# Optimization experiments

Measured on AMD Instinct MI355X. Metric: run time of the kernel, lower is better.

## Reference

```python
import jax, jax.numpy as jnp
import numpy as np
from jax import lax

PRE_NMS = 2000
POST_NMS = 300
NMS_THRESH = 0.7
MIN_SIZE = 16.0
SCALE = 1.0
RATIOS = (0.5, 1.0, 2.0)
SCALES = (8, 16, 32)
STRIDES = (8, 16, 32)
FEAT_HW = ((100, 100), (50, 50), (25, 25))
BASE_SIZE = 16.0


def _anchor_base(scale):
    py = px = BASE_SIZE / 2.0
    ab = np.zeros((len(RATIOS), 4), dtype=np.float32)
    for i, r in enumerate(RATIOS):
        h = BASE_SIZE * scale * np.sqrt(r)
        w = BASE_SIZE * scale * np.sqrt(1.0 / r)
        ab[i] = [py - h / 2.0, px - w / 2.0, py + h / 2.0, px + w / 2.0]
    return ab


def _enum_anchors():
    out = []
    for lvl in range(3):
        ab = _anchor_base(SCALES[lvl])
        hh, ww = FEAT_HW[lvl]
        fs = STRIDES[lvl]
        sy = np.arange(0, hh * fs, fs)
        sx = np.arange(0, ww * fs, fs)
        sx, sy = np.meshgrid(sx, sy)
        shift = np.stack((sy.ravel(), sx.ravel(), sy.ravel(), sx.ravel()), axis=1)
        a = ab[None, :, :] + shift[:, None, :]  # [K, A, 4]
        out.append(a.reshape(-1, 4).astype(np.float32))
    return np.concatenate(out, axis=0)  # [39375, 4]


def setup_inputs() -> dict:
    key = jax.random.key(0)
    ks = jax.random.split(key, 8)
    inp = {
        "feat0": jax.random.normal(ks[0], (2, 256, 100, 100), jnp.float32),
        "feat1": jax.random.normal(ks[1], (2, 256, 50, 50), jnp.float32),
        "feat2": jax.random.normal(ks[2], (2, 256, 25, 25), jnp.float32),
        "conv_w": 0.01 * jax.random.normal(ks[3], (256, 256, 3, 3), jnp.float32),
        "conv_b": jnp.zeros((256,), jnp.float32),
        "score_w": 0.01 * jax.random.normal(ks[4], (6, 256), jnp.float32),
        "score_b": jnp.zeros((6,), jnp.float32),
        "loc_w": 0.01 * jax.random.normal(ks[5], (12, 256), jnp.float32),
        "loc_b": jnp.zeros((12,), jnp.float32),
        "anchors": jnp.asarray(_enum_anchors()),
        "img_h": 800,
        "img_w": 800,
    }
    return inp


def loc2bbox(anchors, loc):
    src_h = anchors[:, 2] - anchors[:, 0]
    src_w = anchors[:, 3] - anchors[:, 1]
    ctr_y = anchors[:, 0] + 0.5 * src_h
    ctr_x = anchors[:, 1] + 0.5 * src_w
    dy, dx, dh, dw = loc[:, 0], loc[:, 1], loc[:, 2], loc[:, 3]
    cy = dy * src_h + ctr_y
    cx = dx * src_w + ctr_x
    h = jnp.exp(dh) * src_h
    w = jnp.exp(dw) * src_w
    return jnp.stack([cy - 0.5 * h, cx - 0.5 * w, cy + 0.5 * h, cx + 0.5 * w], axis=1)


def _iou_matrix(boxes):
    area = (boxes[:, 2] - boxes[:, 0]) * (boxes[:, 3] - boxes[:, 1])
    tl = jnp.maximum(boxes[:, None, :2], boxes[None, :, :2])
    br = jnp.minimum(boxes[:, None, 2:], boxes[None, :, 2:])
    wh = jnp.clip(br - tl, 0.0)
    inter = wh[..., 0] * wh[..., 1]
    return inter / (area[:, None] + area[None, :] - inter + 1e-12)


def _nms_keep(boxes, valid):
    # greedy NMS over score-sorted boxes; returns boolean keep mask
    M = _iou_matrix(boxes)  # [PRE_NMS, PRE_NMS]
    idx = jnp.arange(PRE_NMS)

    def body(i, suppressed):
        sup_later = (~suppressed[i]) & (M[i] > NMS_THRESH) & (idx > i)
        return suppressed | sup_later

    suppressed = lax.fori_loop(0, PRE_NMS, body, ~valid)
    return ~suppressed


def _propose(loc, fg, anchors, img_h, img_w):
    roi = loc2bbox(anchors, loc)  # [S, 4]
    roi = jnp.stack([
        jnp.clip(roi[:, 0], 0.0, float(img_h)),
        jnp.clip(roi[:, 1], 0.0, float(img_w)),
        jnp.clip(roi[:, 2], 0.0, float(img_h)),
        jnp.clip(roi[:, 3], 0.0, float(img_w)),
    ], axis=1)
    hs = roi[:, 2] - roi[:, 0]
    ws = roi[:, 3] - roi[:, 1]
    valid = (hs >= MIN_SIZE * SCALE) & (ws >= MIN_SIZE * SCALE)
    sc = jnp.where(valid, fg, -jnp.inf)
    top_sc, top_idx = lax.top_k(sc, PRE_NMS)
    boxes = roi[top_idx]
    keep = _nms_keep(boxes, jnp.isfinite(top_sc))
    # stable move of kept boxes to the front (indices are unique)
    order = jnp.argsort(jnp.where(keep, jnp.arange(PRE_NMS), PRE_NMS))[:POST_NMS]
    rois = boxes[order] * keep[order][:, None].astype(boxes.dtype)  # zero-pad invalid
    return rois  # [POST_NMS, 4]


def reference(feat0, feat1, feat2, conv_w, conv_b, score_w, score_b, loc_w, loc_b, anchors, img_h, img_w):
    feats = [feat0, feat1, feat2]
    n = feat0.shape[0]
    locs, scores, fgs = [], [], []
    dn = ("NCHW", "OIHW", "NCHW")
    for x in feats:
        h = jax.nn.relu(
            lax.conv_general_dilated(x, conv_w, (1, 1), "SAME", dimension_numbers=dn)
            + conv_b[None, :, None, None]
        )
        hh, ww = h.shape[2], h.shape[3]
        loc = jnp.einsum("nchw,oc->nhwo", h, loc_w) + loc_b  # [n,h,w,12]
        sc = jnp.einsum("nchw,oc->nhwo", h, score_w) + score_b  # [n,h,w,6]
        fg = jax.nn.softmax(sc.reshape(n, hh, ww, 3, 2), axis=-1)[..., 1]
        locs.append(loc.reshape(n, -1, 4))
        scores.append(sc.reshape(n, -1, 2))
        fgs.append(fg.reshape(n, -1))
    rpn_locs = jnp.concatenate(locs, axis=1)      # [n, S, 4]
    rpn_scores = jnp.concatenate(scores, axis=1)  # [n, S, 2]
    rpn_fg = jnp.concatenate(fgs, axis=1)         # [n, S]
    rois = jax.vmap(lambda l, f: _propose(l, f, anchors, img_h, img_w))(rpn_locs, rpn_fg)
    rois = rois.reshape(-1, 4)  # [n*POST_NMS, 4]
    roi_indices = jnp.repeat(jnp.arange(n, dtype=jnp.int32), POST_NMS)
    return rpn_locs, rpn_scores, rois, roi_indices, anchors
```

## Files before the change

kernel.cpp:

```cpp
#include <hip/hip_runtime.h>
#include <hip/hip_fp16.h>
#include <cstdint>
#include <cstddef>

typedef unsigned long long u64;
typedef unsigned int u32;
typedef __attribute__((ext_vector_type(8))) _Float16 f16x8;
typedef __attribute__((ext_vector_type(4))) float f32x4;

#define NANCHORS 39375
#define PRE_NMS  2000
#define POST_NMS 300
#define CAND_CAP 4096
#define MPAD 2048
#define UNEG 0x007FFFFFu

__device__ __forceinline__ u32 f2u(float f) {
  u32 u = __float_as_uint(f);
  return (u & 0x80000000u) ? ~u : (u | 0x80000000u);
}

#define GLOAD16(gp, lp) __builtin_amdgcn_global_load_lds( \
    (const __attribute__((address_space(1))) u32*)(const void*)(gp), \
    (__attribute__((address_space(3))) u32*)(void*)(lp), 16, 0, 0)

__global__ __launch_bounds__(256) void xsplit_kernel(
    const float* __restrict__ f0, const float* __restrict__ f1, const float* __restrict__ f2,
    short* __restrict__ xh, short* __restrict__ xl)
{
  __shared__ float tile[64][65];
  int t = blockIdx.x;
  int HW, W, W2, np; const float* fp; int AB, ABS;
  if (t < 1256)      { HW = 10000; W = 100; W2 = 102; np = 157; fp = f0; AB = 0;       ABS = 2663424; }
  else if (t < 1576) { t -= 1256; HW = 2500; W = 50; W2 = 52; np = 40; fp = f1; AB = 5326848; ABS = 692224; }
  else               { t -= 1576; HW = 625;  W = 25; W2 = 27; np = 10; fp = f2; AB = 6711296; ABS = 186624; }
  int posb = t % np, r = t / np;
  int ci0 = (r & 3) * 64, b = r >> 2;
  int pos0 = posb * 64;
  int tid = threadIdx.x, lane = tid & 63, w = tid >> 6;
  int rp = pos0 + lane; if (rp >= HW) rp = HW - 1;
  const float* src = fp + (size_t)(b * 256 + ci0) * HW;
#pragma unroll
  for (int p = 0; p < 16; ++p) {
    int cl = w * 16 + p;
    tile[cl][lane] = src[(size_t)cl * HW + rp];
  }
  __syncthreads();
  int pix = tid >> 2, cq = tid & 3;
  int pos = pos0 + pix;
  if (pos < HW) {
    int y = pos / W, x = pos - y * W;
    size_t ob = (size_t)AB + (size_t)b * ABS + ((size_t)((y + 1) * W2 + (x + 1))) * 256 + ci0 + cq * 16;
    __align__(16) short hs[16], ls[16];
#pragma unroll
    for (int j = 0; j < 16; ++j) {
      float v = tile[cq * 16 + j][pix];
      __half h = __float2half(v);
      __half l = __float2half((v - __half2float(h)) * 2048.0f);
      hs[j] = __half_as_short(h);
      ls[j] = __half_as_short(l);
    }
    *(int4*)(xh + ob) = ((int4*)hs)[0];
    *(int4*)(xh + ob + 8) = ((int4*)hs)[1];
    *(int4*)(xl + ob) = ((int4*)ls)[0];
    *(int4*)(xl + ob + 8) = ((int4*)ls)[1];
  }
}

__global__ __launch_bounds__(256) void wsplit_kernel(
    const float* __restrict__ w, short* __restrict__ wh, short* __restrict__ wl)
{
  int idx = blockIdx.x * 256 + threadIdx.x;
  int tap = idx >> 16, co = (idx >> 8) & 255, ci = idx & 255;
  float v = w[(size_t)co * 2304 + ci * 9 + tap];
  __half h = __float2half(v);
  __half l = __float2half((v - __half2float(h)) * 2048.0f);
  wh[idx] = __half_as_short(h);
  wl[idx] = __half_as_short(l);
}

__global__ __launch_bounds__(256, 2) void gemmconv_kernel(
    const short* __restrict__ xh, const short* __restrict__ xl,
    const short* __restrict__ wh, const short* __restrict__ wl,
    const float* __restrict__ bias, float* __restrict__ hbase)
{
  __shared__ __align__(16) short smem[32768];

  int lb = (blockIdx.x & 7) * 52 + (blockIdx.x >> 3);
  int HW, W, W2, AB, ABS; size_t hoff;
  if (lb < 316)      { HW = 10000; W = 100; W2 = 102; AB = 0;       ABS = 2663424; hoff = 0; }
  else if (lb < 396) { lb -= 316; HW = 2500; W = 50; W2 = 52; AB = 5326848; ABS = 692224; hoff = 5120000; }
  else               { lb -= 396; HW = 625;  W = 25; W2 = 27; AB = 6711296; ABS = 186624; hoff = 6400000; }
  int mb = lb >> 2, b = (lb >> 1) & 1, nb = lb & 1;
  int pos0 = mb * 128, co0 = nb * 128;

  int tid = threadIdx.x;
  int s = tid & 7, mrow = tid >> 3;
  int aoff[4], boff[4];
#pragma unroll
  for (int i = 0; i < 4; ++i) {
    int m = i * 32 + mrow;
    int pos = pos0 + m; if (pos >= HW) pos = HW - 1;
    int y = pos / W, x = pos - y * W;
    aoff[i] = AB + b * ABS + (y * W2 + x) * 256 + ((s ^ (m & 7)) << 3);
    boff[i] = ((co0 + m) << 8) + ((s ^ (m & 7)) << 3);
  }
  int wv = tid >> 6, lane = tid & 63;
  int lr = lane & 15, lk = lane >> 4;
  int wr = wv >> 1, wc = wv & 1;
  int rA0 = wr * 64 + lr, rB0 = wc * 64 + lr;
  int cs = (lr & 7) << 4;
  int c0 = ((lk * 16) ^ cs) >> 1;
  int c1 = ((64 + lk * 16) ^ cs) >> 1;

  f32x4 acc1[4][4], acc2[4][4];
  f32x4 zro = {0.f, 0.f, 0.f, 0.f};
#pragma unroll
  for (int i = 0; i < 4; ++i)
#pragma unroll
    for (int j = 0; j < 4; ++j) { acc1[i][j] = zro; acc2[i][j] = zro; }

  for (int cc = 0; cc < 36; ++cc) {
    int tap = cc >> 2, cq = cc & 3;
    int ty = tap / 3, tx = tap - ty * 3;
    int adel = (ty * W2 + tx) * 256 + (cq << 6);
    int bdel = (tap << 16) + (cq << 6);
    if (cc) __syncthreads();
#pragma unroll
    for (int i = 0; i < 4; ++i) {
      int d = i * 2048 + wv * 512;
      GLOAD16(xh + aoff[i] + adel, smem + d);
      GLOAD16(xl + aoff[i] + adel, smem + 8192 + d);
      GLOAD16(wh + boff[i] + bdel, smem + 16384 + d);
      GLOAD16(wl + boff[i] + bdel, smem + 24576 + d);
    }
    __syncthreads();
#pragma unroll
    for (int k2 = 0; k2 < 2; ++k2) {
      int ck = k2 ? c1 : c0;
      f16x8 ah[4], al[4], bh[4], bl[4];
#pragma unroll
      for (int q = 0; q < 4; ++q) {
        int ro = (rA0 + q * 16) * 64 + ck;
        ah[q] = *(const f16x8*)(smem + ro);
        al[q] = *(const f16x8*)(smem + 8192 + ro);
        int rb = (rB0 + q * 16) * 64 + ck;
        bh[q] = *(const f16x8*)(smem + 16384 + rb);
        bl[q] = *(const f16x8*)(smem + 24576 + rb);
      }
#pragma unroll
      for (int m4 = 0; m4 < 4; ++m4)
#pragma unroll
        for (int n4 = 0; n4 < 4; ++n4) {
          acc1[m4][n4] = __builtin_amdgcn_mfma_f32_16x16x32_f16(ah[m4], bh[n4], acc1[m4][n4], 0, 0, 0);
          acc2[m4][n4] = __builtin_amdgcn_mfma_f32_16x16x32_f16(ah[m4], bl[n4], acc2[m4][n4], 0, 0, 0);
          acc2[m4][n4] = __builtin_amdgcn_mfma_f32_16x16x32_f16(al[m4], bh[n4], acc2[m4][n4], 0, 0, 0);
        }
    }
  }

  float br[4];
#pragma unroll
  for (int n4 = 0; n4 < 4; ++n4) br[n4] = bias[co0 + wc * 64 + n4 * 16 + lr];
  float* outb = hbase + hoff + (size_t)b * HW * 256;
#pragma unroll
  for (int m4 = 0; m4 < 4; ++m4) {
#pragma unroll
    for (int j = 0; j < 4; ++j) {
      int pos = pos0 + wr * 64 + m4 * 16 + lk * 4 + j;
      if (pos < HW) {
        float* op = outb + (size_t)pos * 256 + co0 + wc * 64 + lr;
#pragma unroll
        for (int n4 = 0; n4 < 4; ++n4)
          op[n4 * 16] = acc1[m4][n4][j] + acc2[m4][n4][j] * 4.8828125e-4f + br[n4];
      }
    }
  }
}

__global__ __launch_bounds__(256) void head_kernel(
    const float* __restrict__ hbase, const float* __restrict__ loc_w, const float* __restrict__ loc_b,
    const float* __restrict__ score_w, const float* __restrict__ score_b,
    const float* __restrict__ anchors, const int* __restrict__ imgh, const int* __restrict__ imgw,
    float* __restrict__ out_locs, float* __restrict__ out_scores,
    float* __restrict__ boxes, u32* __restrict__ ukey)
{
  __shared__ float wT[4 * 1288];
  int tid = threadIdx.x;
  for (int idx = tid; idx < 4608; idx += 256) {
    int o = idx >> 8, c = idx & 255;
    float v = (o < 12) ? loc_w[o * 256 + c] : score_w[(o - 12) * 256 + c];
    wT[(c >> 6) * 1288 + (c & 63) * 20 + o] = v;
  }
  for (int idx = tid; idx < 512; idx += 256) {
    int c = idx >> 1, o = 18 + (idx & 1);
    wT[(c >> 6) * 1288 + (c & 63) * 20 + o] = 0.f;
  }
  __syncthreads();

  int t = blockIdx.x;
  int b = t / 207, r = t % 207;
  int HW, pos0, base_row; size_t hoff;
  if (r < 157)      { HW = 10000; pos0 = r * 64;         base_row = 0;     hoff = 0; }
  else if (r < 197) { HW = 2500;  pos0 = (r - 157) * 64; base_row = 30000; hoff = 5120000; }
  else              { HW = 625;   pos0 = (r - 197) * 64; base_row = 37500; hoff = 6400000; }

  int px = tid >> 2, q = tid & 3;
  int pos = pos0 + px;
  int pc = (pos < HW) ? pos : HW - 1;
  const float* hp = hbase + hoff + ((size_t)b * HW + pc) * 256 + q * 64;
  const float* wq = wT + q * 1288;

  f32x4 acc[5];
#pragma unroll
  for (int o4 = 0; o4 < 5; ++o4) acc[o4] = (f32x4){0.f, 0.f, 0.f, 0.f};

#pragma unroll 4
  for (int i = 0; i < 16; ++i) {
    float4 hv = *(const float4*)(hp + i * 4);
    float hk[4] = {fmaxf(hv.x, 0.f), fmaxf(hv.y, 0.f), fmaxf(hv.z, 0.f), fmaxf(hv.w, 0.f)};
#pragma unroll
    for (int k = 0; k < 4; ++k) {
      const float4* wrow = (const float4*)(wq + (i * 4 + k) * 20);
#pragma unroll
      for (int o4 = 0; o4 < 5; ++o4) {
        float4 wv = wrow[o4];
        acc[o4][0] = fmaf(hk[k], wv.x, acc[o4][0]);
        acc[o4][1] = fmaf(hk[k], wv.y, acc[o4][1]);
        acc[o4][2] = fmaf(hk[k], wv.z, acc[o4][2]);
        acc[o4][3] = fmaf(hk[k], wv.w, acc[o4][3]);
      }
    }
  }
#pragma unroll
  for (int o4 = 0; o4 < 5; ++o4)
#pragma unroll
    for (int cpo = 0; cpo < 4; ++cpo) {
      float v = acc[o4][cpo];
      v += __shfl_xor(v, 1, 64);
      v += __shfl_xor(v, 2, 64);
      acc[o4][cpo] = v;
    }

  if (q == 0 && pos < HW) {
    float sarr[18] = {acc[0][0], acc[0][1], acc[0][2], acc[0][3],
                      acc[1][0], acc[1][1], acc[1][2], acc[1][3],
                      acc[2][0], acc[2][1], acc[2][2], acc[2][3],
                      acc[3][0], acc[3][1], acc[3][2], acc[3][3],
                      acc[4][0], acc[4][1]};
    float IH = (float)(*imgh), IW = (float)(*imgw);
#pragma unroll
    for (int a = 0; a < 3; ++a) {
      float l0 = sarr[4 * a + 0] + loc_b[4 * a + 0];
      float l1 = sarr[4 * a + 1] + loc_b[4 * a + 1];
      float l2 = sarr[4 * a + 2] + loc_b[4 * a + 2];
      float l3 = sarr[4 * a + 3] + loc_b[4 * a + 3];
      float sc0 = sarr[12 + 2 * a + 0] + score_b[2 * a + 0];
      float sc1 = sarr[12 + 2 * a + 1] + score_b[2 * a + 1];

      int row = base_row + pos * 3 + a;
      size_t g = (size_t)b * NANCHORS + row;
      *(float4*)(out_locs + g * 4) = make_float4(l0, l1, l2, l3);
      out_scores[g * 2 + 0] = sc0; out_scores[g * 2 + 1] = sc1;

      float mx = fmaxf(sc0, sc1);
      float e0 = expf(sc0 - mx), e1 = expf(sc1 - mx);
      float fg = e1 / (e0 + e1);

      const float* an = anchors + (size_t)row * 4;
      float a0 = an[0], a1 = an[1], a2 = an[2], a3 = an[3];
      float sh = a2 - a0, sw = a3 - a1;
      float cy = a0 + 0.5f * sh, cx = a1 + 0.5f * sw;
      float ncy = l0 * sh + cy, ncx = l1 * sw + cx;
      float nh = expf(l2) * sh, nw = expf(l3) * sw;
      float y1 = fminf(fmaxf(ncy - 0.5f * nh, 0.f), IH);
      float x1 = fminf(fmaxf(ncx - 0.5f * nw, 0.f), IW);
      float y2 = fminf(fmaxf(ncy + 0.5f * nh, 0.f), IH);
      float x2 = fminf(fmaxf(ncx + 0.5f * nw, 0.f), IW);
      bool valid = ((y2 - y1) >= 16.0f) && ((x2 - x1) >= 16.0f);
      float scm = valid ? fg : -__builtin_inff();

      *(float4*)(boxes + g * 4) = make_float4(y1, x1, y2, x2);
      ukey[g] = f2u(scm);
    }
  }
}

__global__ void copyf_kernel(const float* __restrict__ a, float* __restrict__ o, int n) {
  int t = blockIdx.x * 256 + threadIdx.x;
  if (t < n) o[t] = a[t];
}

__global__ __launch_bounds__(1024) void selectsort_kernel(
    const u32* __restrict__ ukey, const float* __restrict__ boxes,
    float* __restrict__ topbox, u64* __restrict__ sup0)
{
  int b = blockIdx.x, tid = threadIdx.x;
  int lane = tid & 63;
  const u32* u = ukey + (size_t)b * NANCHORS;
  __shared__ u32 hist[256];
  __shared__ u32 sh_prefix;
  __shared__ int sh_rem;
  __shared__ int sh_cnt;
  __shared__ u64 key[CAND_CAP];
  __shared__ unsigned char validf[2048];

  u32 val[39];
#pragma unroll
  for (int k = 0; k < 38; ++k) val[k] = u[tid + k * 1024];
  val[38] = (tid < 463) ? u[tid + 38912] : 0u;

  u32 prefix = 0; int rem = PRE_NMS;
#pragma unroll 1
  for (int pass = 0; pass < 4; ++pass) {
    int shift = 24 - 8 * pass;
    if (tid < 256) hist[tid] = 0;
    __syncthreads();
    u32 himask = (pass == 0) ? 0u : (0xFFFFFFFFu << (shift + 8));
    u32 pmask = prefix & himask;
#pragma unroll
    for (int k = 0; k < 39; ++k) {
      bool live = (k < 38) || (tid < 463);
      u32 v = val[k];
      bool m = live && ((v & himask) == pmask);
      u32 bin = (v >> shift) & 255u;
      u64 actm = __ballot(m);
      if (actm) {
        int src = __ffsll(actm) - 1;
        u32 binf = __shfl(bin, src, 64);
        bool same = m && (bin == binf);
        u64 sm = __ballot(same);
        if (same) {
          if (lane == __ffsll(sm) - 1)
            atomicAdd(&hist[binf], (u32)__popcll(sm));
        } else if (m) {
          atomicAdd(&hist[bin], 1u);
        }
      }
    }
    __syncthreads();
    if (tid < 64) {
      u32 h0 = hist[4 * lane], h1 = hist[4 * lane + 1];
      u32 h2 = hist[4 * lane + 2], h3 = hist[4 * lane + 3];
      u32 L = h0 + h1 + h2 + h3;
      u32 SS = L;
#pragma unroll
      for (int off = 1; off < 64; off <<= 1) {
        u32 tv = __shfl_down(SS, off, 64);
        if (lane + off < 64) SS += tv;
      }
      u32 T = SS - L;
      u32 s3 = h3 + T, s2 = h2 + s3, s1 = h1 + s2, s0 = h0 + s1;
      u32 sv[5] = {s0, s1, s2, s3, T};
#pragma unroll
      for (int j = 0; j < 4; ++j) {
        if ((int)sv[j] >= rem && (int)sv[j + 1] < rem) {
          sh_prefix = prefix | ((u32)(4 * lane + j) << shift);
          sh_rem = rem - (int)sv[j + 1];
        }
      }
    }
    __syncthreads();
    prefix = sh_prefix; rem = sh_rem;
  }

  if (tid == 0) sh_cnt = 0;
  __syncthreads();
#pragma unroll
  for (int k = 0; k < 39; ++k) {
    bool live = (k < 38) || (tid < 463);
    u32 v = val[k];
    bool c = live && (v >= prefix);
    u64 mask = __ballot(c);
    if (mask) {
      int leader = __ffsll(mask) - 1;
      int cntw = __popcll(mask);
      int base = 0;
      if (lane == leader) base = atomicAdd(&sh_cnt, cntw);
      base = __shfl(base, leader, 64);
      int p = base + (int)__popcll(mask & ((1ull << lane) - 1ull));
      if (c && p < CAND_CAP)
        key[p] = ((u64)v << 32) | (u32)(~(u32)(tid + k * 1024));
    }
  }
  __syncthreads();
  int cnt = (sh_cnt < CAND_CAP) ? sh_cnt : CAND_CAP;
  for (int t = tid; t < CAND_CAP; t += 1024)
    if (t >= cnt) key[t] = 0ull;
  __syncthreads();

  u32 n = (cnt <= 2048) ? 2048u : (u32)CAND_CAP;
  for (u32 k = 2; k <= n; k <<= 1) {
    for (u32 j = k >> 1; j > 0; j >>= 1) {
      __syncthreads();
      for (u32 t = tid; t < n; t += 1024) {
        u32 ixj = t ^ j;
        if (ixj > t) {
          u64 a = key[t], c = key[ixj];
          bool desc = ((t & k) == 0);
          if (desc ? (a < c) : (a > c)) { key[t] = c; key[ixj] = a; }
        }
      }
    }
  }
  __syncthreads();

  for (int t = tid; t < 2048; t += 1024) {
    unsigned char vf = 0;
    if (t < PRE_NMS) {
      u64 kk = key[t];
      u32 uu = (u32)(kk >> 32);
      float* tb = topbox + ((size_t)b * PRE_NMS + t) * 4;
      if (uu != 0u) {
        u32 idx = ~((u32)kk);
        const float* bp = boxes + ((size_t)b * NANCHORS + idx) * 4;
        tb[0] = bp[0]; tb[1] = bp[1]; tb[2] = bp[2]; tb[3] = bp[3];
        vf = (uu != UNEG) ? 1 : 0;
      } else {
        tb[0] = 0.f; tb[1] = 0.f; tb[2] = 0.f; tb[3] = 0.f;
      }
    }
    validf[t] = vf;
  }
  __syncthreads();
  if (tid < 32) {
    u64 m = 0;
    for (int bit = 0; bit < 64; ++bit) {
      int j = tid * 64 + bit;
      if (j >= PRE_NMS || !validf[j]) m |= (1ull << bit);
    }
    sup0[b * 32 + tid] = m;
  }
}

__global__ __launch_bounds__(256) void iou_kernel(const float* __restrict__ topbox, u32* __restrict__ M32)
{
  int t = blockIdx.x * 256 + threadIdx.x;
  int b = blockIdx.y;
  int w = t / 2000, i = t % 2000;
  const float* tb = topbox + (size_t)b * PRE_NMS * 4;
  const float* bi = tb + (size_t)i * 4;
  float iy1 = bi[0], ix1 = bi[1], iy2 = bi[2], ix2 = bi[3];
  float ai = (iy2 - iy1) * (ix2 - ix1);
  u64 m = 0;
  for (int bit = 0; bit < 64; ++bit) {
    int j = w * 64 + bit;
    if (j < PRE_NMS && j > i) {
      const float* bj = tb + (size_t)j * 4;
      float ty = fmaxf(iy1, bj[0]), tx = fmaxf(ix1, bj[1]);
      float by = fminf(iy2, bj[2]), bx = fminf(ix2, bj[3]);
      float hh = fmaxf(by - ty, 0.f), ww = fmaxf(bx - tx, 0.f);
      float inter = hh * ww;
      float aj = (bj[2] - bj[0]) * (bj[3] - bj[1]);
      float iou = inter / (ai + aj - inter + 1e-12f);
      if (iou > 0.7f) m |= (1ull << bit);
    }
  }
  u32* out = M32 + (size_t)b * MPAD * 64;
  out[(size_t)(2 * w)     * MPAD + i] = (u32)m;
  out[(size_t)(2 * w + 1) * MPAD + i] = (u32)(m >> 32);
}

__global__ __launch_bounds__(320) void final_kernel(
    const u32* __restrict__ M32, const u64* __restrict__ sup0, const float* __restrict__ topbox,
    float* __restrict__ rois, float* __restrict__ roiidx)
{
  int b = blockIdx.x, tid = threadIdx.x;
  __shared__ u32 supl[64];
  __shared__ int ord[POST_NMS];
  __shared__ int cnt_s;

  if (tid < 64) {
    int l = tid;
    const u32* col = M32 + (size_t)b * MPAD * 64 + (size_t)l * MPAD;
    u32 sup = ((const u32*)sup0)[b * 64 + l];
    uint4 A[16], B[16];
#pragma unroll
    for (int k = 0; k < 16; ++k) A[k] = *(const uint4*)(col + 4 * k);

#define NMS_PROC(buf, cc) do {                                                     \
  _Pragma("unroll")                                                                \
  for (int rr = 0; rr < 64; ++rr) {                                                \
    u32 d = ((rr & 3) == 0) ? buf[rr >> 2].x : ((rr & 3) == 1) ? buf[rr >> 2].y :  \
            ((rr & 3) == 2) ? buf[rr >> 2].z : buf[rr >> 2].w;                     \
    u32 sb = (u32)__builtin_amdgcn_readlane((int)sup, 2 * (cc) + (rr >> 5));       \
    u32 m = ((sb >> (rr & 31)) & 1u) - 1u;                                         \
    sup |= m & d;                                                                  \
  } } while (0)

    for (int c = 0; c < 32; c += 2) {
#pragma unroll
      for (int k = 0; k < 16; ++k) B[k] = *(const uint4*)(col + (c + 1) * 64 + 4 * k);
      NMS_PROC(A, c);
      if (c + 2 < 32) {
#pragma unroll
        for (int k = 0; k < 16; ++k) A[k] = *(const uint4*)(col + (c + 2) * 64 + 4 * k);
      }
      NMS_PROC(B, c + 1);
    }
    supl[l] = sup;
  }
  __syncthreads();
  if (tid == 0) {
    int cnt = 0;
    for (int w = 0; w < 64 && cnt < POST_NMS; ++w) {
      u32 kept = ~supl[w];
      while (kept && cnt < POST_NMS) {
        int bit = __builtin_ctz(kept); kept &= kept - 1;
        ord[cnt++] = w * 32 + bit;
      }
    }
    cnt_s = cnt;
  }
  __syncthreads();
  if (tid < POST_NMS) {
    float v0 = 0.f, v1 = 0.f, v2 = 0.f, v3 = 0.f;
    if (tid < cnt_s) {
      const float* tb = topbox + ((size_t)b * PRE_NMS + ord[tid]) * 4;
      v0 = tb[0]; v1 = tb[1]; v2 = tb[2]; v3 = tb[3];
    }
    float* r = rois + ((size_t)b * POST_NMS + tid) * 4;
    r[0] = v0; r[1] = v1; r[2] = v2; r[3] = v3;
    roiidx[b * POST_NMS + tid] = (float)b;
  }
}

extern "C" void kernel_launch(void* const* d_in, const int* in_sizes, int n_in,
                              void* d_out, int out_size, void* d_ws, size_t ws_size,
                              hipStream_t stream) {
  const float* feat0   = (const float*)d_in[0];
  const float* feat1   = (const float*)d_in[1];
  const float* feat2   = (const float*)d_in[2];
  const float* conv_w  = (const float*)d_in[3];
  const float* conv_b  = (const float*)d_in[4];
  const float* score_w = (const float*)d_in[5];
  const float* score_b = (const float*)d_in[6];
  const float* loc_w   = (const float*)d_in[7];
  const float* loc_b   = (const float*)d_in[8];
  const float* anchors = (const float*)d_in[9];
  const int*   img_h   = (const int*)d_in[10];
  const int*   img_w   = (const int*)d_in[11];

  float* out_f       = (float*)d_out;
  float* out_locs    = out_f;
  float* out_scores  = out_f + 315000;
  float* out_rois    = out_f + 472500;
  float* out_roiidx  = out_f + 474900;
  float* out_anchors = out_f + 475500;

  char* p = (char*)d_ws;
  float* hb = (float*)p;      p += (size_t)6720000 * 4;
  short* xth = (short*)p;     p += (size_t)7084544 * 2;
  short* xtl = (short*)p;     p += (size_t)7084544 * 2;
  short* wsh = (short*)p;     p += (size_t)589824 * 2;
  short* wsl = (short*)p;     p += (size_t)589824 * 2;
  float* boxes = (float*)p;   p += (size_t)315000 * 4;
  u32* ukey = (u32*)p;        p += (size_t)78752 * 4;
  float* topbox = (float*)p;  p += (size_t)16000 * 4;
  u32* M32 = (u32*)p;         p += (size_t)2 * MPAD * 64 * 4;
  u64* sup0 = (u64*)p;        p += 64 * 8;

  hipMemsetAsync(xth, 0, (size_t)7084544 * 4, stream);
  xsplit_kernel<<<1656, 256, 0, stream>>>(feat0, feat1, feat2, xth, xtl);
  wsplit_kernel<<<2304, 256, 0, stream>>>(conv_w, wsh, wsl);
  gemmconv_kernel<<<416, 256, 0, stream>>>(xth, xtl, wsh, wsl, conv_b, hb);
  head_kernel<<<414, 256, 0, stream>>>(
      hb, loc_w, loc_b, score_w, score_b, anchors, img_h, img_w,
      out_locs, out_scores, boxes, ukey);
  copyf_kernel<<<(157500 + 255) / 256, 256, 0, stream>>>(anchors, out_anchors, 157500);
  selectsort_kernel<<<2, 1024, 0, stream>>>(ukey, boxes, topbox, sup0);
  iou_kernel<<<dim3(250, 2), 256, 0, stream>>>(topbox, M32);
  final_kernel<<<2, 320, 0, stream>>>(M32, sup0, topbox, out_rois, out_roiidx);
}
```

Measured before the change: 361.4 us.

## Fuse 1x1 head projection into conv GEMM epilogue and zero only padding ring

```diff
diff --git a/kernel.cpp b/kernel.cpp
--- a/kernel.cpp
+++ b/kernel.cpp
@@ -14,6 +14,7 @@
 #define CAND_CAP 4096
 #define MPAD 2048
 #define UNEG 0x007FFFFFu
+#define NPIX 26250
 
 __device__ __forceinline__ u32 f2u(float f) {
   u32 u = __float_as_uint(f);
@@ -23,6 +24,30 @@
 #define GLOAD16(gp, lp) __builtin_amdgcn_global_load_lds( \
     (const __attribute__((address_space(1))) u32*)(const void*)(gp), \
     (__attribute__((address_space(3))) u32*)(void*)(lp), 16, 0, 0)
+
+#define DPP_SUM16(v) do { \
+  v += __int_as_float(__builtin_amdgcn_update_dpp(0, __float_as_int(v), 0x128, 0xf, 0xf, true)); \
+  v += __int_as_float(__builtin_amdgcn_update_dpp(0, __float_as_int(v), 0x124, 0xf, 0xf, true)); \
+  v += __int_as_float(__builtin_amdgcn_update_dpp(0, __float_as_int(v), 0x122, 0xf, 0xf, true)); \
+  v += __int_as_float(__builtin_amdgcn_update_dpp(0, __float_as_int(v), 0x121, 0xf, 0xf, true)); \
+} while (0)
+
+__global__ __launch_bounds__(64) void ringzero_kernel(short* __restrict__ xh, short* __restrict__ xl) {
+  int t = blockIdx.x;
+  int b = t / 712, i = t % 712;
+  int W2, AB, ABS;
+  if (i < 404)      { W2 = 102; AB = 0;       ABS = 2663424; }
+  else if (i < 608) { i -= 404; W2 = 52; AB = 5326848; ABS = 692224; }
+  else              { i -= 608; W2 = 27; AB = 6711296; ABS = 186624; }
+  int y, x;
+  if (i < W2)          { y = 0;      x = i; }
+  else if (i < 2 * W2) { y = W2 - 1; x = i - W2; }
+  else { int j = i - 2 * W2; y = 1 + (j >> 1); x = (j & 1) ? (W2 - 1) : 0; }
+  size_t base = (size_t)AB + (size_t)b * ABS + ((size_t)(y * W2 + x)) * 256 + threadIdx.x * 4;
+  int2 z = {0, 0};
+  *(int2*)(xh + base) = z;
+  *(int2*)(xl + base) = z;
+}
 
 __global__ __launch_bounds__(256) void xsplit_kernel(
     const float* __restrict__ f0, const float* __restrict__ f1, const float* __restrict__ f2,
@@ -82,15 +107,17 @@
 __global__ __launch_bounds__(256, 2) void gemmconv_kernel(
     const short* __restrict__ xh, const short* __restrict__ xl,
     const short* __restrict__ wh, const short* __restrict__ wl,
-    const float* __restrict__ bias, float* __restrict__ hbase)
+    const float* __restrict__ bias,
+    const float* __restrict__ loc_w, const float* __restrict__ score_w,
+    float* __restrict__ proj2)
 {
   __shared__ __align__(16) short smem[32768];
 
   int lb = (blockIdx.x & 7) * 52 + (blockIdx.x >> 3);
-  int HW, W, W2, AB, ABS; size_t hoff;
-  if (lb < 316)      { HW = 10000; W = 100; W2 = 102; AB = 0;       ABS = 2663424; hoff = 0; }
-  else if (lb < 396) { lb -= 316; HW = 2500; W = 50; W2 = 52; AB = 5326848; ABS = 692224; hoff = 5120000; }
-  else               { lb -= 396; HW = 625;  W = 25; W2 = 27; AB = 6711296; ABS = 186624; hoff = 6400000; }
+  int HW, W, W2, AB, ABS, lvlbase;
+  if (lb < 316)      { HW = 10000; W = 100; W2 = 102; AB = 0;       ABS = 2663424; lvlbase = 0; }
+  else if (lb < 396) { lb -= 316; HW = 2500; W = 50; W2 = 52; AB = 5326848; ABS = 692224; lvlbase = 10000; }
+  else               { lb -= 396; HW = 625;  W = 25; W2 = 27; AB = 6711296; ABS = 186624; lvlbase = 12500; }
   int mb = lb >> 2, b = (lb >> 1) & 1, nb = lb & 1;
   int pos0 = mb * 128, co0 = nb * 128;
 
@@ -162,127 +189,105 @@
   float br[4];
 #pragma unroll
   for (int n4 = 0; n4 < 4; ++n4) br[n4] = bias[co0 + wc * 64 + n4 * 16 + lr];
-  float* outb = hbase + hoff + (size_t)b * HW * 256;
-#pragma unroll
-  for (int m4 = 0; m4 < 4; ++m4) {
-#pragma unroll
-    for (int j = 0; j < 4; ++j) {
-      int pos = pos0 + wr * 64 + m4 * 16 + lk * 4 + j;
-      if (pos < HW) {
-        float* op = outb + (size_t)pos * 256 + co0 + wc * 64 + lr;
-#pragma unroll
-        for (int n4 = 0; n4 < 4; ++n4)
-          op[n4 * 16] = acc1[m4][n4][j] + acc2[m4][n4][j] * 4.8828125e-4f + br[n4];
-      }
-    }
-  }
-}
-
-__global__ __launch_bounds__(256) void head_kernel(
-    const float* __restrict__ hbase, const float* __restrict__ loc_w, const float* __restrict__ loc_b,
-    const float* __restrict__ score_w, const float* __restrict__ score_b,
+  float* pslot = proj2 + (size_t)(nb * 2 + wc) * NPIX * 20;
+  int Pbase = b * 13125 + lvlbase;
+
+#pragma unroll 1
+  for (int half = 0; half < 2; ++half) {
+    float wpr[4][9];
+#pragma unroll
+    for (int n4 = 0; n4 < 4; ++n4) {
+      int c = co0 + wc * 64 + n4 * 16 + lr;
+#pragma unroll
+      for (int oo = 0; oo < 9; ++oo) {
+        int o = half * 9 + oo;
+        wpr[n4][oo] = (o < 12) ? loc_w[o * 256 + c] : score_w[(o - 12) * 256 + c];
+      }
+    }
+#pragma unroll
+    for (int m4 = 0; m4 < 4; ++m4) {
+#pragma unroll
+      for (int j = 0; j < 4; ++j) {
+        int pos = pos0 + wr * 64 + m4 * 16 + lk * 4 + j;
+        bool ok = pos < HW;
+        float po[9];
+#pragma unroll
+        for (int oo = 0; oo < 9; ++oo) po[oo] = 0.f;
+#pragma unroll
+        for (int n4 = 0; n4 < 4; ++n4) {
+          float h = acc1[m4][n4][j] + acc2[m4][n4][j] * 4.8828125e-4f + br[n4];
+          h = ok ? fmaxf(h, 0.f) : 0.f;
+#pragma unroll
+          for (int oo = 0; oo < 9; ++oo) po[oo] = fmaf(h, wpr[n4][oo], po[oo]);
+        }
+#pragma unroll
+        for (int oo = 0; oo < 9; ++oo) DPP_SUM16(po[oo]);
+        if (ok && lr < 9) {
+          float out = po[0];
+#pragma unroll
+          for (int oo = 1; oo < 9; ++oo) if (lr == oo) out = po[oo];
+          pslot[(size_t)(Pbase + pos) * 20 + half * 9 + lr] = out;
+        }
+      }
+    }
+  }
+}
+
+__global__ __launch_bounds__(256) void decode_kernel(
+    const float* __restrict__ proj2, const float* __restrict__ loc_b, const float* __restrict__ score_b,
     const float* __restrict__ anchors, const int* __restrict__ imgh, const int* __restrict__ imgw,
     float* __restrict__ out_locs, float* __restrict__ out_scores,
     float* __restrict__ boxes, u32* __restrict__ ukey)
 {
-  __shared__ float wT[4 * 1288];
-  int tid = threadIdx.x;
-  for (int idx = tid; idx < 4608; idx += 256) {
-    int o = idx >> 8, c = idx & 255;
-    float v = (o < 12) ? loc_w[o * 256 + c] : score_w[(o - 12) * 256 + c];
-    wT[(c >> 6) * 1288 + (c & 63) * 20 + o] = v;
-  }
-  for (int idx = tid; idx < 512; idx += 256) {
-    int c = idx >> 1, o = 18 + (idx & 1);
-    wT[(c >> 6) * 1288 + (c & 63) * 20 + o] = 0.f;
-  }
-  __syncthreads();
-
-  int t = blockIdx.x;
-  int b = t / 207, r = t % 207;
-  int HW, pos0, base_row; size_t hoff;
-  if (r < 157)      { HW = 10000; pos0 = r * 64;         base_row = 0;     hoff = 0; }
-  else if (r < 197) { HW = 2500;  pos0 = (r - 157) * 64; base_row = 30000; hoff = 5120000; }
-  else              { HW = 625;   pos0 = (r - 197) * 64; base_row = 37500; hoff = 6400000; }
-
-  int px = tid >> 2, q = tid & 3;
-  int pos = pos0 + px;
-  int pc = (pos < HW) ? pos : HW - 1;
-  const float* hp = hbase + hoff + ((size_t)b * HW + pc) * 256 + q * 64;
-  const float* wq = wT + q * 1288;
-
-  f32x4 acc[5];
-#pragma unroll
-  for (int o4 = 0; o4 < 5; ++o4) acc[o4] = (f32x4){0.f, 0.f, 0.f, 0.f};
-
-#pragma unroll 4
-  for (int i = 0; i < 16; ++i) {
-    float4 hv = *(const float4*)(hp + i * 4);
-    float hk[4] = {fmaxf(hv.x, 0.f), fmaxf(hv.y, 0.f), fmaxf(hv.z, 0.f), fmaxf(hv.w, 0.f)};
-#pragma unroll
-    for (int k = 0; k < 4; ++k) {
-      const float4* wrow = (const float4*)(wq + (i * 4 + k) * 20);
-#pragma unroll
-      for (int o4 = 0; o4 < 5; ++o4) {
-        float4 wv = wrow[o4];
-        acc[o4][0] = fmaf(hk[k], wv.x, acc[o4][0]);
-        acc[o4][1] = fmaf(hk[k], wv.y, acc[o4][1]);
-        acc[o4][2] = fmaf(hk[k], wv.z, acc[o4][2]);
-        acc[o4][3] = fmaf(hk[k], wv.w, acc[o4][3]);
-      }
-    }
-  }
-#pragma unroll
-  for (int o4 = 0; o4 < 5; ++o4)
-#pragma unroll
-    for (int cpo = 0; cpo < 4; ++cpo) {
-      float v = acc[o4][cpo];
-      v += __shfl_xor(v, 1, 64);
-      v += __shfl_xor(v, 2, 64);
-      acc[o4][cpo] = v;
-    }
-
-  if (q == 0 && pos < HW) {
-    float sarr[18] = {acc[0][0], acc[0][1], acc[0][2], acc[0][3],
-                      acc[1][0], acc[1][1], acc[1][2], acc[1][3],
-                      acc[2][0], acc[2][1], acc[2][2], acc[2][3],
-                      acc[3][0], acc[3][1], acc[3][2], acc[3][3],
-                      acc[4][0], acc[4][1]};
-    float IH = (float)(*imgh), IW = (float)(*imgw);
-#pragma unroll
-    for (int a = 0; a < 3; ++a) {
-      float l0 = sarr[4 * a + 0] + loc_b[4 * a + 0];
-      float l1 = sarr[4 * a + 1] + loc_b[4 * a + 1];
-      float l2 = sarr[4 * a + 2] + loc_b[4 * a + 2];
-      float l3 = sarr[4 * a + 3] + loc_b[4 * a + 3];
-      float sc0 = sarr[12 + 2 * a + 0] + score_b[2 * a + 0];
-      float sc1 = sarr[12 + 2 * a + 1] + score_b[2 * a + 1];
-
-      int row = base_row + pos * 3 + a;
-      size_t g = (size_t)b * NANCHORS + row;
-      *(float4*)(out_locs + g * 4) = make_float4(l0, l1, l2, l3);
-      out_scores[g * 2 + 0] = sc0; out_scores[g * 2 + 1] = sc1;
-
-      float mx = fmaxf(sc0, sc1);
-      float e0 = expf(sc0 - mx), e1 = expf(sc1 - mx);
-      float fg = e1 / (e0 + e1);
-
-      const float* an = anchors + (size_t)row * 4;
-      float a0 = an[0], a1 = an[1], a2 = an[2], a3 = an[3];
-      float sh = a2 - a0, sw = a3 - a1;
-      float cy = a0 + 0.5f * sh, cx = a1 + 0.5f * sw;
-      float ncy = l0 * sh + cy, ncx = l1 * sw + cx;
-      float nh = expf(l2) * sh, nw = expf(l3) * sw;
-      float y1 = fminf(fmaxf(ncy - 0.5f * nh, 0.f), IH);
-      float x1 = fminf(fmaxf(ncx - 0.5f * nw, 0.f), IW);
-      float y2 = fminf(fmaxf(ncy + 0.5f * nh, 0.f), IH);
-      float x2 = fminf(fmaxf(ncx + 0.5f * nw, 0.f), IW);
-      bool valid = ((y2 - y1) >= 16.0f) && ((x2 - x1) >= 16.0f);
-      float scm = valid ? fg : -__builtin_inff();
-
-      *(float4*)(boxes + g * 4) = make_float4(y1, x1, y2, x2);
-      ukey[g] = f2u(scm);
-    }
+  int P = blockIdx.x * 256 + threadIdx.x;
+  if (P >= NPIX) return;
+  int b = P / 13125, r = P % 13125;
+  int pos, base_row;
+  if (r < 10000)      { pos = r;         base_row = 0; }
+  else if (r < 12500) { pos = r - 10000; base_row = 30000; }
+  else                { pos = r - 12500; base_row = 37500; }
+
+  float sarr[18];
+#pragma unroll
+  for (int o = 0; o < 18; ++o)
+    sarr[o] = proj2[(size_t)P * 20 + o] + proj2[(size_t)NPIX * 20 + (size_t)P * 20 + o]
+            + proj2[(size_t)2 * NPIX * 20 + (size_t)P * 20 + o]
+            + proj2[(size_t)3 * NPIX * 20 + (size_t)P * 20 + o];
+
+  float IH = (float)(*imgh), IW = (float)(*imgw);
+#pragma unroll
+  for (int a = 0; a < 3; ++a) {
+    float l0 = sarr[4 * a + 0] + loc_b[4 * a + 0];
+    float l1 = sarr[4 * a + 1] + loc_b[4 * a + 1];
+    float l2 = sarr[4 * a + 2] + loc_b[4 * a + 2];
+    float l3 = sarr[4 * a + 3] + loc_b[4 * a + 3];
+    float sc0 = sarr[12 + 2 * a + 0] + score_b[2 * a + 0];
+    float sc1 = sarr[12 + 2 * a + 1] + score_b[2 * a + 1];
+
+    int row = base_row + pos * 3 + a;
+    size_t g = (size_t)b * NANCHORS + row;
+    *(float4*)(out_locs + g * 4) = make_float4(l0, l1, l2, l3);
+    out_scores[g * 2 + 0] = sc0; out_scores[g * 2 + 1] = sc1;
+
+    float mx = fmaxf(sc0, sc1);
+    float e0 = expf(sc0 - mx), e1 = expf(sc1 - mx);
+    float fg = e1 / (e0 + e1);
+
+    const float* an = anchors + (size_t)row * 4;
+    float a0 = an[0], a1 = an[1], a2 = an[2], a3 = an[3];
+    float sh = a2 - a0, sw = a3 - a1;
+    float cy = a0 + 0.5f * sh, cx = a1 + 0.5f * sw;
+    float ncy = l0 * sh + cy, ncx = l1 * sw + cx;
+    float nh = expf(l2) * sh, nw = expf(l3) * sw;
+    float y1 = fminf(fmaxf(ncy - 0.5f * nh, 0.f), IH);
+    float x1 = fminf(fmaxf(ncx - 0.5f * nw, 0.f), IW);
+    float y2 = fminf(fmaxf(ncy + 0.5f * nh, 0.f), IH);
+    float x2 = fminf(fmaxf(ncx + 0.5f * nw, 0.f), IW);
+    bool valid = ((y2 - y1) >= 16.0f) && ((x2 - x1) >= 16.0f);
+    float scm = valid ? fg : -__builtin_inff();
+
+    *(float4*)(boxes + g * 4) = make_float4(y1, x1, y2, x2);
+    ukey[g] = f2u(scm);
   }
 }
 
@@ -549,23 +554,23 @@
   float* out_anchors = out_f + 475500;
 
   char* p = (char*)d_ws;
-  float* hb = (float*)p;      p += (size_t)6720000 * 4;
   short* xth = (short*)p;     p += (size_t)7084544 * 2;
   short* xtl = (short*)p;     p += (size_t)7084544 * 2;
   short* wsh = (short*)p;     p += (size_t)589824 * 2;
   short* wsl = (short*)p;     p += (size_t)589824 * 2;
+  float* proj2 = (float*)p;   p += (size_t)4 * NPIX * 20 * 4;
   float* boxes = (float*)p;   p += (size_t)315000 * 4;
   u32* ukey = (u32*)p;        p += (size_t)78752 * 4;
   float* topbox = (float*)p;  p += (size_t)16000 * 4;
   u32* M32 = (u32*)p;         p += (size_t)2 * MPAD * 64 * 4;
   u64* sup0 = (u64*)p;        p += 64 * 8;
 
-  hipMemsetAsync(xth, 0, (size_t)7084544 * 4, stream);
+  ringzero_kernel<<<1424, 64, 0, stream>>>(xth, xtl);
   xsplit_kernel<<<1656, 256, 0, stream>>>(feat0, feat1, feat2, xth, xtl);
   wsplit_kernel<<<2304, 256, 0, stream>>>(conv_w, wsh, wsl);
-  gemmconv_kernel<<<416, 256, 0, stream>>>(xth, xtl, wsh, wsl, conv_b, hb);
-  head_kernel<<<414, 256, 0, stream>>>(
-      hb, loc_w, loc_b, score_w, score_b, anchors, img_h, img_w,
+  gemmconv_kernel<<<416, 256, 0, stream>>>(xth, xtl, wsh, wsl, conv_b, loc_w, score_w, proj2);
+  decode_kernel<<<(NPIX + 255) / 256, 256, 0, stream>>>(
+      proj2, loc_b, score_b, anchors, img_h, img_w,
       out_locs, out_scores, boxes, ukey);
   copyf_kernel<<<(157500 + 255) / 256, 256, 0, stream>>>(anchors, out_anchors, 157500);
   selectsort_kernel<<<2, 1024, 0, stream>>>(ukey, boxes, topbox, sup0);
```

New measurement: 362.9 us. No clear change (+0.4%).
